# Kernel optimization log

Hardware: AMD Instinct MI355X
Metric: run time of the kernel (lower is better)

## Reference

```python
import jax, jax.numpy as jnp
import numpy as np

N, D = 8192, 512
NUM_SOURCES = 8


def setup_inputs() -> dict:
    key = jax.random.key(0)
    k1, k2, k3 = jax.random.split(key, 3)
    image_features = jax.random.normal(k1, (N, D), dtype=jnp.float32)
    text_features = jax.random.normal(k2, (N, D), dtype=jnp.float32)
    logit_scale = jnp.ones((), dtype=jnp.float32)
    source_labels = jax.random.randint(k3, (N,), 0, NUM_SOURCES, dtype=jnp.int64)
    return {
        "image_features": image_features,
        "text_features": text_features,
        "logit_scale": logit_scale,
        "source_labels": source_labels,
    }


def reference(image_features, text_features, logit_scale, source_labels):
    n = source_labels.shape[0]
    # [N, N] logits and row-wise log-softmax
    logits = logit_scale * (image_features @ text_features.T)
    log_probs = jax.nn.log_softmax(logits, axis=1)
    # same-source mask, diagonal excluded
    mask = (source_labels[:, None] == source_labels[None, :]) & (~jnp.eye(n, dtype=bool))
    count_pos = mask.sum(axis=1)  # [N]
    row_sum = jnp.where(mask, log_probs, 0.0).sum(axis=1)  # [N]
    # per-row mean over positives; rows with zero positives contribute 0
    row_mean = jnp.where(count_pos > 0, row_sum / jnp.maximum(count_pos, 1).astype(log_probs.dtype), 0.0)
    # loss = -(sum_i row_mean_i) / N
    return -row_mean.sum() / n
```

## Files before the change

### kernel.cpp

```cpp
#include <hip/hip_runtime.h>
#include <cmath>

#define NN 8192
#define DD 512
#define NSRC 8
#define PSW 8
#define COFF 100.0f

typedef __bf16 bf16x8 __attribute__((ext_vector_type(8)));
typedef float  f32x4  __attribute__((ext_vector_type(4)));

__device__ __forceinline__ unsigned short f2bf(float f) {
    unsigned u = __float_as_uint(f);
    u += 0x7fffu + ((u >> 16) & 1u);
    return (unsigned short)(u >> 16);
}

__global__ __launch_bounds__(256) void k_prep(
    const float* __restrict__ img, const float* __restrict__ txt,
    const int* __restrict__ labels,
    unsigned short* __restrict__ imgB, unsigned short* __restrict__ txtB,
    float* __restrict__ Tsum, int* __restrict__ counts,
    float* __restrict__ dsv)
{
    const int tid = threadIdx.x;
    if (blockIdx.x >= 128) {
        const int wv   = tid >> 6;
        const int lane = tid & 63;
        const int row  = (blockIdx.x - 128) * 4 + wv;
        const size_t base = (size_t)row * DD + lane * 8;
        const float4 i0 = *(const float4*)(img + base);
        const float4 i1 = *(const float4*)(img + base + 4);
        const float4 t0 = *(const float4*)(txt + base);
        const float4 t1 = *(const float4*)(txt + base + 4);
        union { unsigned short s[8]; uint4 v; } oi, ot;
        oi.s[0] = f2bf(i0.x); oi.s[1] = f2bf(i0.y); oi.s[2] = f2bf(i0.z); oi.s[3] = f2bf(i0.w);
        oi.s[4] = f2bf(i1.x); oi.s[5] = f2bf(i1.y); oi.s[6] = f2bf(i1.z); oi.s[7] = f2bf(i1.w);
        ot.s[0] = f2bf(t0.x); ot.s[1] = f2bf(t0.y); ot.s[2] = f2bf(t0.z); ot.s[3] = f2bf(t0.w);
        ot.s[4] = f2bf(t1.x); ot.s[5] = f2bf(t1.y); ot.s[6] = f2bf(t1.z); ot.s[7] = f2bf(t1.w);
        *(uint4*)(imgB + base) = oi.v;
        *(uint4*)(txtB + base) = ot.v;
        float ds = i0.x * t0.x + i0.y * t0.y + i0.z * t0.z + i0.w * t0.w
                 + i1.x * t1.x + i1.y * t1.y + i1.z * t1.z + i1.w * t1.w;
#pragma unroll
        for (int off = 32; off; off >>= 1) ds += __shfl_xor(ds, off);
        if (lane == 0) dsv[row] = ds;
        return;
    }
    __shared__ float Tacc[NSRC * DD];
    __shared__ int cacc[NSRC];
    const int d0 = 2 * tid;
#pragma unroll
    for (int s = 0; s < NSRC; s++) {
        Tacc[s * DD + d0] = 0.f;
        Tacc[s * DD + d0 + 1] = 0.f;
    }
    if (tid < NSRC) cacc[tid] = 0;
    __syncthreads();

    const int row0 = blockIdx.x * 64;
    if (tid < 64) atomicAdd(&cacc[labels[row0 + tid]], 1);

    for (int j = 0; j < 64; j++) {
        const int lab = labels[row0 + j];
        const float2 v = *(const float2*)(txt + (size_t)(row0 + j) * DD + d0);
        Tacc[lab * DD + d0]     += v.x;
        Tacc[lab * DD + d0 + 1] += v.y;
    }
    __syncthreads();
#pragma unroll
    for (int k = 0; k < NSRC * DD / 256; k++) {
        const int e = k * 256 + tid;
        atomicAdd(&Tsum[e], Tacc[e]);
    }
    if (tid < NSRC) atomicAdd(&counts[tid], cacc[tid]);
}

__global__ __launch_bounds__(512, 2) void k_lse_mfma256(
    const unsigned short* __restrict__ imgB, const unsigned short* __restrict__ txtB,
    const float* __restrict__ scale_p, float* __restrict__ ps)
{
    __shared__ uint4 lds[8192];
    const float scale = scale_p[0];
    const int tid  = threadIdx.x;
    const int lane = tid & 63;
    const int w    = tid >> 6;
    const int wr   = w >> 1;
    const int wc   = w & 1;
    const int lq   = lane >> 4;
    const int ln   = lane & 15;
    const int c    = blockIdx.x & 7;
    const int l    = blockIdx.x >> 3;
    const int by   = c * 4 + (l >> 3);
    const int bcg  = l & 7;
    const int row0    = by * 256;
    const int colBase = bcg * 1024;

    const int st_r  = tid >> 3;
    const int st_kc = (tid & 7) ^ (st_r & 7);
    const int xsw   = ln & 7;

    int aA[2][2], aB[2][2];
#pragma unroll
    for (int b = 0; b < 2; b++)
#pragma unroll
        for (int ks = 0; ks < 2; ks++) {
            const int perm = ((ks << 2) + lq) ^ xsw;
            aA[b][ks] = b * 65536 + ((wr * 64 + ln) * 8 + perm) * 16;
            aB[b][ks] = b * 65536 + 32768 + ((wc * 128 + ln) * 8 + perm) * 16;
        }
    const unsigned short* gA0 = imgB + (size_t)(row0 + st_r) * DD + (st_kc << 3);
    const unsigned short* gB0 = txtB + (size_t)(colBase + st_r) * DD + (st_kc << 3);

#define SA(BUF, Q, T)                                                          \
    { const unsigned short* g = gA0 + ((Q) << 15) + (((T) & 7) << 6);          \
      __builtin_amdgcn_global_load_lds(                                        \
          (const __attribute__((address_space(1))) void*)g,                    \
          (__attribute__((address_space(3))) void*)                            \
              &lds[(BUF) * 4096 + (Q) * 512 + tid], 16, 0, 0); }
#define SB(BUF, Q, T)                                                          \
    { const unsigned short* g = gB0 + ((size_t)(((T) >> 3) & 3) << 17)         \
          + ((Q) << 15) + (((T) & 7) << 6);                                    \
      __builtin_amdgcn_global_load_lds(                                        \
          (const __attribute__((address_space(1))) void*)g,                    \
          (__attribute__((address_space(3))) void*)                            \
              &lds[(BUF) * 4096 + 2048 + (Q) * 512 + tid], 16, 0, 0); }

#define PH_(BUF, HALF, STG, VM)                                                \
    do {                                                                       \
        if (!(HALF)) {                                                         \
            _Pragma("unroll") for (int ks = 0; ks < 2; ks++)                   \
                _Pragma("unroll") for (int ii = 0; ii < 4; ii++)               \
                    af[ii][ks] = *reinterpret_cast<const bf16x8*>(             \
                        (const char*)lds + aA[BUF][ks] + ii * 2048);           \
        }                                                                      \
        bf16x8 bf[2][2][2];                                                    \
        _Pragma("unroll") for (int ks = 0; ks < 2; ks++)                       \
            _Pragma("unroll") for (int j2 = 0; j2 < 2; j2++)                   \
                _Pragma("unroll") for (int jj = 0; jj < 2; jj++)               \
                    bf[j2][jj][ks] = *reinterpret_cast<const bf16x8*>(         \
                        (const char*)lds + aB[BUF][ks]                         \
                        + ((HALF) * 2 + j2) * 4096 + jj * 2048);               \
        STG;                                                                   \
        __builtin_amdgcn_s_barrier();                                          \
        asm volatile("s_waitcnt lgkmcnt(0)" ::: "memory");                     \
        __builtin_amdgcn_sched_barrier(0);                                     \
        __builtin_amdgcn_s_setprio(1);                                         \
        _Pragma("unroll") for (int ks = 0; ks < 2; ks++) {                     \
            _Pragma("unroll") for (int ii = 0; ii < 4; ii++) {                 \
                _Pragma("unroll") for (int j2 = 0; j2 < 2; j2++) {             \
                    _Pragma("unroll") for (int jj = 0; jj < 2; jj++) {         \
                        acc[ii][((HALF) * 2 + j2) * 2 + jj] =                  \
                            __builtin_amdgcn_mfma_f32_16x16x32_bf16(           \
                                af[ii][ks], bf[j2][jj][ks],                    \
                                acc[ii][((HALF) * 2 + j2) * 2 + jj], 0, 0, 0); \
                    }                                                          \
                }                                                              \
            }                                                                  \
        }                                                                      \
        __builtin_amdgcn_s_setprio(0);                                         \
        if (VM) { asm volatile("s_waitcnt vmcnt(2)" ::: "memory"); }           \
        __builtin_amdgcn_s_barrier();                                          \
    } while (0)

#pragma unroll
    for (int q = 0; q < 4; q++) SA(0, q, 0);
#pragma unroll
    for (int q = 0; q < 4; q++) SB(0, q, 0);
    SA(1, 0, 1); SA(1, 2, 1);
    asm volatile("s_waitcnt vmcnt(2)" ::: "memory");
    __builtin_amdgcn_s_barrier();

    f32x4 acc[4][8];
    f32x4 s_run[4];
#pragma unroll
    for (int i = 0; i < 4; i++) {
        s_run[i] = (f32x4){0.f, 0.f, 0.f, 0.f};
#pragma unroll
        for (int j = 0; j < 8; j++) acc[i][j] = (f32x4){0.f, 0.f, 0.f, 0.f};
    }
    bf16x8 af[4][2];

#pragma unroll 1
    for (int v0 = 0; v0 < 32; v0 += 2) {
        PH_(0, 0,
            SA(1, 1, v0 + 1); SA(1, 3, v0 + 1);
            SB(1, 0, v0 + 1); SB(1, 1, v0 + 1);
            SB(1, 2, v0 + 1); SB(1, 3, v0 + 1), 0);
        PH_(0, 1, SA(0, 0, v0 + 2); SA(0, 2, v0 + 2), 1);
        PH_(1, 0,
            SA(0, 1, v0 + 2); SA(0, 3, v0 + 2);
            SB(0, 0, v0 + 2); SB(0, 1, v0 + 2);
            SB(0, 2, v0 + 2); SB(0, 3, v0 + 2), 0);
        PH_(1, 1, SA(1, 0, v0 + 3); SA(1, 2, v0 + 3), 1);
        if ((v0 & 6) == 6) {
#pragma unroll
            for (int i = 0; i < 4; i++) {
#pragma unroll
                for (int rg = 0; rg < 4; rg++) {
                    float es = s_run[i][rg];
#pragma unroll
                    for (int j = 0; j < 8; j++)
                        es += __expf(fmaf(acc[i][j][rg], scale, -COFF));
                    s_run[i][rg] = es;
                }
#pragma unroll
                for (int j = 0; j < 8; j++)
                    acc[i][j] = (f32x4){0.f, 0.f, 0.f, 0.f};
            }
        }
    }

    asm volatile("s_waitcnt vmcnt(0)" ::: "memory");
    __syncthreads();

    float* fred = (float*)lds;
#pragma unroll
    for (int i = 0; i < 4; i++) {
#pragma unroll
        for (int rg = 0; rg < 4; rg++) {
            float es = s_run[i][rg];
#pragma unroll
            for (int off = 8; off; off >>= 1) es += __shfl_xor(es, off);
            if (ln == 0)
                fred[(wr * 64 + i * 16 + lq * 4 + rg) * 2 + wc] = es;
        }
    }
    __syncthreads();
    if (tid < 256) {
        const float tot = fred[tid * 2] + fred[tid * 2 + 1];
        ps[(size_t)(row0 + tid) * PSW + bcg] = tot;
    }
#undef SA
#undef SB
#undef PH_
}

__global__ __launch_bounds__(256) void k_finalize(
    const unsigned short* __restrict__ imgB,
    const int* __restrict__ labels, const float* __restrict__ scale_p,
    const float* __restrict__ Tsum, const int* __restrict__ counts,
    const float* __restrict__ ps, const float* __restrict__ dsv,
    float* __restrict__ out)
{
    const float scale = scale_p[0];
    const int tid = threadIdx.x;
    const int lane = tid & 63;
    const int wave = tid >> 6;
    const int rowBase = blockIdx.x * 16 + wave * 4;
    float local = 0.f;
#pragma unroll
    for (int it = 0; it < 4; it++) {
        const int i = rowBase + it;
        const int lab = labels[i];
        const float* sp = Tsum + lab * DD + lane * 8;
        union { uint4 v; unsigned short s[8]; } iv;
        iv.v = *(const uint4*)(imgB + (size_t)i * DD + lane * 8);
        const float4 s0 = *(const float4*)(sp);
        const float4 s1 = *(const float4*)(sp + 4);
        float dt = 0.f;
        dt = fmaf(__uint_as_float((unsigned)iv.s[0] << 16), s0.x, dt);
        dt = fmaf(__uint_as_float((unsigned)iv.s[1] << 16), s0.y, dt);
        dt = fmaf(__uint_as_float((unsigned)iv.s[2] << 16), s0.z, dt);
        dt = fmaf(__uint_as_float((unsigned)iv.s[3] << 16), s0.w, dt);
        dt = fmaf(__uint_as_float((unsigned)iv.s[4] << 16), s1.x, dt);
        dt = fmaf(__uint_as_float((unsigned)iv.s[5] << 16), s1.y, dt);
        dt = fmaf(__uint_as_float((unsigned)iv.s[6] << 16), s1.z, dt);
        dt = fmaf(__uint_as_float((unsigned)iv.s[7] << 16), s1.w, dt);
        float es = (lane < PSW) ? ps[(size_t)i * PSW + lane] : 0.f;
#pragma unroll
        for (int off = 32; off; off >>= 1) {
            dt += __shfl_xor(dt, off);
            es += __shfl_xor(es, off);
        }
        if (lane == 0) {
            const float lse = COFF + __logf(es);
            const int cnt = counts[lab] - 1;
            if (cnt > 0) {
                const float row_sum = scale * (dt - dsv[i]) - (float)cnt * lse;
                local += row_sum / (float)cnt;
            }
        }
    }
    __shared__ float red[4];
    if (lane == 0) red[wave] = local;
    __syncthreads();
    if (tid == 0) {
        const float t = red[0] + red[1] + red[2] + red[3];
        atomicAdd(out, -t / (float)NN);
    }
}

extern "C" void kernel_launch(void* const* d_in, const int* in_sizes, int n_in,
                              void* d_out, int out_size, void* d_ws, size_t ws_size,
                              hipStream_t stream)
{
    const float* img     = (const float*)d_in[0];
    const float* txt     = (const float*)d_in[1];
    const float* scale_p = (const float*)d_in[2];
    const int*   labels  = (const int*)d_in[3];
    float* out = (float*)d_out;

    char* ws = (char*)d_ws;
    float* ps    = (float*)(ws);
    float* Tsum  = (float*)(ws + (1 << 18));
    int*   counts = (int*)(ws + (1 << 18) + NSRC * DD * 4);
    float* dsv   = (float*)(ws + 0x48000);
    unsigned short* imgB = (unsigned short*)(ws + 2 * 1024 * 1024);
    unsigned short* txtB = (unsigned short*)(ws + 10 * 1024 * 1024);

    hipMemsetAsync(ws + (1 << 18), 0, NSRC * DD * 4 + 64, stream);
    hipMemsetAsync(d_out, 0, 4, stream);

    k_prep<<<128 + NN / 4, 256, 0, stream>>>(
        img, txt, labels, imgB, txtB, Tsum, counts, dsv);
    k_lse_mfma256<<<256, 512, 0, stream>>>(imgB, txtB, scale_p, ps);
    k_finalize<<<NN / 16, 256, 0, stream>>>(imgB, labels, scale_p,
                                            Tsum, counts, ps, dsv, out);
}
```

Measured before the change: 158.6 us.

## Split GEMM phases into finer sub-phases and drop redundant barriers

Each half-phase of the bf16 MFMA main loop is split into two sub-phases, each loading only two B fragments per k-step. This lowers register pressure and lets LDS reads interleave more finely with MFMAs. The per-phase s_barrier pairs and the explicit lgkmcnt(0) waits are removed, leaving two barriers per buffer placed where A/B reuse requires them, with the compiler now inserting the LDS waits. The risk is weaker control over the LDS/global load schedule and possible stalls from compiler-chosen waitcnts.

```diff
diff --git a/kernel.cpp b/kernel.cpp
--- a/kernel.cpp
+++ b/kernel.cpp
@@ -106,8 +106,8 @@
 #pragma unroll
         for (int ks = 0; ks < 2; ks++) {
             const int perm = ((ks << 2) + lq) ^ xsw;
-            aA[b][ks] = b * 65536 + ((wr * 64 + ln) * 8 + perm) * 16;
-            aB[b][ks] = b * 65536 + 32768 + ((wc * 128 + ln) * 8 + perm) * 16;
+            aA[b][ks] = b * 65536 + (wr * 64 + ln) * 128 + perm * 16;
+            aB[b][ks] = b * 65536 + 32768 + (wc * 128 + ln) * 128 + perm * 16;
         }
     const unsigned short* gA0 = imgB + (size_t)(row0 + st_r) * DD + (st_kc << 3);
     const unsigned short* gB0 = txtB + (size_t)(colBase + st_r) * DD + (st_kc << 3);
@@ -126,41 +126,33 @@
           (__attribute__((address_space(3))) void*)                            \
               &lds[(BUF) * 4096 + 2048 + (Q) * 512 + tid], 16, 0, 0); }
 
-#define PH_(BUF, HALF, STG, VM)                                                \
+#define PH_(BUF, JH, RA, STG)                                                  \
     do {                                                                       \
-        if (!(HALF)) {                                                         \
+        if (RA) {                                                              \
             _Pragma("unroll") for (int ks = 0; ks < 2; ks++)                   \
                 _Pragma("unroll") for (int ii = 0; ii < 4; ii++)               \
                     af[ii][ks] = *reinterpret_cast<const bf16x8*>(             \
                         (const char*)lds + aA[BUF][ks] + ii * 2048);           \
         }                                                                      \
-        bf16x8 bf[2][2][2];                                                    \
+        bf16x8 bf[2][2];                                                       \
         _Pragma("unroll") for (int ks = 0; ks < 2; ks++)                       \
-            _Pragma("unroll") for (int j2 = 0; j2 < 2; j2++)                   \
-                _Pragma("unroll") for (int jj = 0; jj < 2; jj++)               \
-                    bf[j2][jj][ks] = *reinterpret_cast<const bf16x8*>(         \
-                        (const char*)lds + aB[BUF][ks]                         \
-                        + ((HALF) * 2 + j2) * 4096 + jj * 2048);               \
+            _Pragma("unroll") for (int jj = 0; jj < 2; jj++)                   \
+                bf[jj][ks] = *reinterpret_cast<const bf16x8*>(                 \
+                    (const char*)lds + aB[BUF][ks] + (JH) * 4096 + jj * 2048); \
         STG;                                                                   \
-        __builtin_amdgcn_s_barrier();                                          \
-        asm volatile("s_waitcnt lgkmcnt(0)" ::: "memory");                     \
         __builtin_amdgcn_sched_barrier(0);                                     \
         __builtin_amdgcn_s_setprio(1);                                         \
         _Pragma("unroll") for (int ks = 0; ks < 2; ks++) {                     \
             _Pragma("unroll") for (int ii = 0; ii < 4; ii++) {                 \
-                _Pragma("unroll") for (int j2 = 0; j2 < 2; j2++) {             \
-                    _Pragma("unroll") for (int jj = 0; jj < 2; jj++) {         \
-                        acc[ii][((HALF) * 2 + j2) * 2 + jj] =                  \
-                            __builtin_amdgcn_mfma_f32_16x16x32_bf16(           \
-                                af[ii][ks], bf[j2][jj][ks],                    \
-                                acc[ii][((HALF) * 2 + j2) * 2 + jj], 0, 0, 0); \
-                    }                                                          \
+                _Pragma("unroll") for (int jj = 0; jj < 2; jj++) {             \
+                    acc[ii][(JH) * 2 + jj] =                                   \
+                        __builtin_amdgcn_mfma_f32_16x16x32_bf16(               \
+                            af[ii][ks], bf[jj][ks], acc[ii][(JH) * 2 + jj],    \
+                            0, 0, 0);                                          \
                 }                                                              \
             }                                                                  \
         }                                                                      \
         __builtin_amdgcn_s_setprio(0);                                         \
-        if (VM) { asm volatile("s_waitcnt vmcnt(2)" ::: "memory"); }           \
-        __builtin_amdgcn_s_barrier();                                          \
     } while (0)
 
 #pragma unroll
@@ -183,16 +175,26 @@
 
 #pragma unroll 1
     for (int v0 = 0; v0 < 32; v0 += 2) {
-        PH_(0, 0,
+        PH_(0, 0, 1,
             SA(1, 1, v0 + 1); SA(1, 3, v0 + 1);
             SB(1, 0, v0 + 1); SB(1, 1, v0 + 1);
-            SB(1, 2, v0 + 1); SB(1, 3, v0 + 1), 0);
-        PH_(0, 1, SA(0, 0, v0 + 2); SA(0, 2, v0 + 2), 1);
-        PH_(1, 0,
+            SB(1, 2, v0 + 1); SB(1, 3, v0 + 1));
+        PH_(0, 1, 0, (void)0);
+        __builtin_amdgcn_s_barrier();
+        PH_(0, 2, 0, SA(0, 0, v0 + 2); SA(0, 2, v0 + 2));
+        PH_(0, 3, 0, (void)0);
+        asm volatile("s_waitcnt vmcnt(2)" ::: "memory");
+        __builtin_amdgcn_s_barrier();
+        PH_(1, 0, 1,
             SA(0, 1, v0 + 2); SA(0, 3, v0 + 2);
             SB(0, 0, v0 + 2); SB(0, 1, v0 + 2);
-            SB(0, 2, v0 + 2); SB(0, 3, v0 + 2), 0);
-        PH_(1, 1, SA(1, 0, v0 + 3); SA(1, 2, v0 + 3), 1);
+            SB(0, 2, v0 + 2); SB(0, 3, v0 + 2));
+        PH_(1, 1, 0, (void)0);
+        __builtin_amdgcn_s_barrier();
+        PH_(1, 2, 0, SA(1, 0, v0 + 3); SA(1, 2, v0 + 3));
+        PH_(1, 3, 0, (void)0);
+        asm volatile("s_waitcnt vmcnt(2)" ::: "memory");
+        __builtin_amdgcn_s_barrier();
         if ((v0 & 6) == 6) {
 #pragma unroll
             for (int i = 0; i < 4; i++) {
```

New measurement: 157.4 us. No clear change (-0.8%).
